# Kernel tuning notes

Measured on AMD Instinct MI355X. Metric: run time of the kernel, lower is better.

Reference implementation:

```python
import jax, jax.numpy as jnp
import numpy as np

B, S, H, E, K = 8, 4096, 1024, 256, 64
NEG = -1e30  # finite stand-in for -inf to keep grads NaN-free


def setup_inputs() -> dict:
    key = jax.random.key(0)
    ks = jax.random.split(key, 8)
    Hq = H // 4
    sc = 0.02
    return {
        "hidden_states": jax.random.normal(ks[0], (B, S, H), dtype=jnp.float32),
        "attention_mask": jnp.ones((B, S), dtype=jnp.int32),
        "block_boundaries": jnp.sort(jax.random.randint(ks[1], (B, K), 0, S), axis=-1),
        "tok_w1": jax.random.normal(ks[2], (H, Hq), dtype=jnp.float32) * sc,
        "tok_b1": jnp.zeros((Hq,), dtype=jnp.float32),
        "tok_w2": jax.random.normal(ks[3], (Hq, 1), dtype=jnp.float32) * sc,
        "tok_b2": jnp.zeros((1,), dtype=jnp.float32),
        "blk_w1": jax.random.normal(ks[4], (H, Hq), dtype=jnp.float32) * sc,
        "blk_b1": jnp.zeros((Hq,), dtype=jnp.float32),
        "blk_w2": jax.random.normal(ks[5], (Hq, 1), dtype=jnp.float32) * sc,
        "blk_b2": jnp.zeros((1,), dtype=jnp.float32),
        "out_w": jax.random.normal(ks[6], (H, E), dtype=jnp.float32) * sc,
        "out_b": jnp.zeros((E,), dtype=jnp.float32),
    }


def _attn_scores(x, w1, b1, w2, b2):
    # Linear -> Tanh -> Linear(.,1), squeeze last dim
    return (jnp.tanh(x @ w1 + b1) @ w2 + b2)[..., 0]


def reference(hidden_states, attention_mask, block_boundaries,
              tok_w1, tok_b1, tok_w2, tok_b2,
              blk_w1, blk_b1, blk_w2, blk_b2,
              out_w, out_b):
    Bz, Sz, Hz = hidden_states.shape
    Kz = block_boundaries.shape[1]
    pos = jnp.arange(Sz)
    # token -> block id: last boundary <= pos (tokens before first boundary get -1)
    block_id = jax.vmap(lambda bnd: jnp.searchsorted(bnd, pos, side='right') - 1)(block_boundaries)  # [B,S]
    member = block_id[:, :, None] == jnp.arange(Kz)[None, None, :]      # [B,S,K]
    valid = (attention_mask == 1) & (block_id >= 0)                     # [B,S]
    m_full = member & valid[:, :, None]                                 # [B,S,K]

    # stage 1: per-block masked softmax over tokens
    tok_scores = _attn_scores(hidden_states, tok_w1, tok_b1, tok_w2, tok_b2)  # [B,S]
    s = jnp.where(m_full, tok_scores[:, :, None], NEG)
    mx = jnp.max(s, axis=1, keepdims=True)                              # [B,1,K]
    e = jnp.where(m_full, jnp.exp(tok_scores[:, :, None] - mx), 0.0)
    denom = jnp.sum(e, axis=1, keepdims=True)                           # [B,1,K]
    w = jnp.where(denom > 0, e / jnp.maximum(denom, 1e-30), 0.0)
    block_embed = jnp.einsum('bsk,bsd->bkd', w, hidden_states)          # [B,K,H]
    block_valid = denom[:, 0, :] > 0                                    # [B,K] (empty blocks dropped)

    # stage 2: softmax over (non-empty) blocks
    blk_scores = _attn_scores(block_embed, blk_w1, blk_b1, blk_w2, blk_b2)    # [B,K]
    blk_scores = jnp.where(block_valid, blk_scores, NEG)
    bw = jax.nn.softmax(blk_scores, axis=-1)
    func = jnp.einsum('bk,bkd->bd', bw, block_embed)                    # [B,H]

    out = func @ out_w + out_b                                          # [B,E]
    return out / jnp.maximum(jnp.linalg.norm(out, axis=-1, keepdims=True), 1e-12)
```

## Files before the change

### kernel.cpp

```cpp
#include <hip/hip_runtime.h>
#include <math.h>
#include <limits.h>

#define BB 8
#define SS 4096
#define HH 1024
#define EE 256
#define KK 64
#define HQ 256
#define NEGF -1e30f

typedef short bf16x8 __attribute__((ext_vector_type(8)));
typedef float f32x4  __attribute__((ext_vector_type(4)));

__device__ inline short f2bf(float x) {
    unsigned u = __float_as_uint(x);
    unsigned r = (u + 0x7fffu + ((u >> 16) & 1u)) >> 16;
    return (short)r;
}

__device__ inline unsigned pk2bf(float lo, float hi) {
    unsigned a = __float_as_uint(lo) + 0x8000u;
    unsigned b = __float_as_uint(hi) + 0x8000u;
    return (a >> 16) | (b & 0xffff0000u);
}

__global__ __launch_bounds__(256) void convert_both_kernel(
    const float* __restrict__ tok_w1, const float* __restrict__ blk_w1,
    short* __restrict__ w1s_tok, short* __restrict__ w1s_blk)
{
    const int kb = blockIdx.x & 31, which = blockIdx.x >> 5;
    const float* src = which ? blk_w1 : tok_w1;
    short* dst = which ? w1s_blk : w1s_tok;
    const int n = threadIdx.x;
    for (int kk = 0; kk < 32; kk++)
        dst[kb * 8192 + n * 32 + kk] = f2bf(src[(kb * 32 + kk) * HQ + n]);
}

__global__ __launch_bounds__(256, 4) void mfma_score4_kernel(
    const float* __restrict__ X, const short* __restrict__ w1s,
    const float* __restrict__ b1, const float* __restrict__ w2,
    const float* __restrict__ b2, float* __restrict__ out)
{
    __shared__ __attribute__((aligned(16))) short As[2][1024];
    __shared__ float part[4][32];

    const int t = threadIdx.x;
    const int wv = t >> 6, lane = t & 63, lo = lane & 15, q = lane >> 4;
    const long row0 = (long)blockIdx.x * 32;

    f32x4 acc[2][4];
#pragma unroll
    for (int i = 0; i < 2; i++)
#pragma unroll
        for (int j = 0; j < 4; j++) acc[i][j] = (f32x4){0.f, 0.f, 0.f, 0.f};

    const int c = t >> 1, half = t & 1;
    const int srow = ((c >> 6) << 4) + (c & 15);
    const int skofs = ((c >> 4) & 3) * 8 + half * 4;
    const float* xs = X + (row0 + srow) * HH + skofs;
    short* const dst0 = &As[0][c * 8 + half * 4];
    short* const dst1 = &As[1][c * 8 + half * 4];
    const short* wp = w1s + (wv * 64 + lo) * 32 + q * 8;

    {
        float4 v = *(const float4*)xs;
        unsigned u0 = pk2bf(v.x, v.y), u1 = pk2bf(v.z, v.w);
        ((unsigned*)dst0)[0] = u0; ((unsigned*)dst0)[1] = u1;
    }
    bf16x8 bA[4], bB[4];
#pragma unroll
    for (int ct = 0; ct < 4; ct++)
        bA[ct] = *(const bf16x8*)(wp + ct * 512);
    __syncthreads();

    for (int kb = 0; kb < 32; kb += 2) {
        {
            float4 v = *(const float4*)(xs + (kb + 1) * 32);
#pragma unroll
            for (int ct = 0; ct < 4; ct++)
                bB[ct] = *(const bf16x8*)(wp + (kb + 1) * 8192 + ct * 512);
            bf16x8 af[2];
#pragma unroll
            for (int rt = 0; rt < 2; rt++)
                af[rt] = *(bf16x8*)(&As[0][(rt * 64 + q * 16 + lo) * 8]);
#pragma unroll
            for (int rt = 0; rt < 2; rt++)
#pragma unroll
                for (int ct = 0; ct < 4; ct++)
                    acc[rt][ct] = __builtin_amdgcn_mfma_f32_16x16x32_bf16(
                        af[rt], bA[ct], acc[rt][ct], 0, 0, 0);
            unsigned u0 = pk2bf(v.x, v.y), u1 = pk2bf(v.z, v.w);
            ((unsigned*)dst1)[0] = u0; ((unsigned*)dst1)[1] = u1;
        }
        __syncthreads();
        {
            const int k2 = (kb + 2 < 32) ? kb + 2 : 31;
            float4 v = *(const float4*)(xs + k2 * 32);
#pragma unroll
            for (int ct = 0; ct < 4; ct++)
                bA[ct] = *(const bf16x8*)(wp + k2 * 8192 + ct * 512);
            bf16x8 af[2];
#pragma unroll
            for (int rt = 0; rt < 2; rt++)
                af[rt] = *(bf16x8*)(&As[1][(rt * 64 + q * 16 + lo) * 8]);
#pragma unroll
            for (int rt = 0; rt < 2; rt++)
#pragma unroll
                for (int ct = 0; ct < 4; ct++)
                    acc[rt][ct] = __builtin_amdgcn_mfma_f32_16x16x32_bf16(
                        af[rt], bB[ct], acc[rt][ct], 0, 0, 0);
            unsigned u0 = pk2bf(v.x, v.y), u1 = pk2bf(v.z, v.w);
            ((unsigned*)dst0)[0] = u0; ((unsigned*)dst0)[1] = u1;
        }
        __syncthreads();
    }

    float rowpart[2][4];
#pragma unroll
    for (int rt = 0; rt < 2; rt++)
#pragma unroll
        for (int r = 0; r < 4; r++) rowpart[rt][r] = 0.f;
#pragma unroll
    for (int ct = 0; ct < 4; ct++) {
        const int cc = wv * 64 + ct * 16 + lo;
        const float b1c = b1[cc], w2c = w2[cc];
#pragma unroll
        for (int rt = 0; rt < 2; rt++)
#pragma unroll
            for (int r = 0; r < 4; r++)
                rowpart[rt][r] += tanhf(acc[rt][ct][r] + b1c) * w2c;
    }
#pragma unroll
    for (int rt = 0; rt < 2; rt++)
#pragma unroll
        for (int r = 0; r < 4; r++) {
            float v = rowpart[rt][r];
            v += __shfl_down(v, 8, 64);
            v += __shfl_down(v, 4, 64);
            v += __shfl_down(v, 2, 64);
            v += __shfl_down(v, 1, 64);
            rowpart[rt][r] = v;
        }
    if (lo == 0)
#pragma unroll
        for (int rt = 0; rt < 2; rt++)
#pragma unroll
            for (int r = 0; r < 4; r++)
                part[wv][rt * 16 + q * 4 + r] = rowpart[rt][r];
    __syncthreads();
    if (t < 32)
        out[row0 + t] = part[0][t] + part[1][t] + part[2][t] + part[3][t] + b2[0];
}

__global__ __launch_bounds__(256) void block_stats_kernel(
    const float* __restrict__ scores, const int* __restrict__ mask,
    const int* __restrict__ bnd, float* __restrict__ bden,
    float* __restrict__ wtok, float* __restrict__ embed)
{
    const int b = blockIdx.x >> 6, k = blockIdx.x & 63;
    const int start = bnd[b * KK + k];
    const int end = (k == KK - 1) ? SS : bnd[b * KK + k + 1];
    const int tid = threadIdx.x;
    __shared__ float r[4];
    __shared__ float mshared, dshared;

    *((float4*)(embed + (long)blockIdx.x * HH) + tid) = (float4){0.f, 0.f, 0.f, 0.f};
    if (k == 0)
        for (int s = tid; s < start; s += 256) wtok[b * SS + s] = 0.f;

    float m = NEGF;
    for (int s = start + tid; s < end; s += 256)
        if (mask[b * SS + s] == 1) m = fmaxf(m, scores[b * SS + s]);
    for (int off = 32; off > 0; off >>= 1) m = fmaxf(m, __shfl_down(m, off, 64));
    if ((tid & 63) == 0) r[tid >> 6] = m;
    __syncthreads();
    if (tid == 0) mshared = fmaxf(fmaxf(r[0], r[1]), fmaxf(r[2], r[3]));
    __syncthreads();
    m = mshared;

    float d = 0.f;
    for (int s = start + tid; s < end; s += 256)
        if (mask[b * SS + s] == 1) d += expf(scores[b * SS + s] - m);
    for (int off = 32; off > 0; off >>= 1) d += __shfl_down(d, off, 64);
    __syncthreads();
    if ((tid & 63) == 0) r[tid >> 6] = d;
    __syncthreads();
    if (tid == 0) {
        float den = r[0] + r[1] + r[2] + r[3];
        bden[blockIdx.x] = den;
        dshared = (den > 0.f) ? 1.f / fmaxf(den, 1e-30f) : 0.f;
    }
    __syncthreads();
    const float inv = dshared;
    for (int s = start + tid; s < end; s += 256)
        wtok[b * SS + s] = (mask[b * SS + s] == 1) ? expf(scores[b * SS + s] - m) * inv : 0.f;
}

#define TCH 16
__global__ __launch_bounds__(256) void block_embed4_kernel(
    const float* __restrict__ hidden, const float* __restrict__ wtok,
    const int* __restrict__ bnd, float* __restrict__ embed)
{
    const int b = blockIdx.x >> 8;
    const int ch = blockIdx.x & 255;
    const int t = threadIdx.x;
    __shared__ int bsh[KK];
    __shared__ float wsh[TCH];
    const int s0 = ch * TCH, s1 = s0 + TCH;
    if (t < KK) bsh[t] = bnd[b * KK + t];
    if (t >= 64 && t < 64 + TCH) wsh[t - 64] = wtok[b * SS + s0 + (t - 64)];
    __syncthreads();

    int cur = -1;
#pragma unroll
    for (int i = 0; i < KK; i++) cur = (bsh[i] <= s0) ? i : cur;
    const int nxt = (cur + 1 < KK) ? bsh[cur + 1] : INT_MAX;

    const float* hr0 = hidden + ((long)b * SS + s0) * HH + t;
    float a0 = 0.f, a1 = 0.f, a2 = 0.f, a3 = 0.f;

    if (nxt >= s1 && cur >= 0) {
#pragma unroll
        for (int i = 0; i < TCH; i++) {
            const float w = wsh[i];
            const float* hr = hr0 + (long)i * HH;
            a0 = fmaf(w, hr[0], a0);
            a1 = fmaf(w, hr[256], a1);
            a2 = fmaf(w, hr[512], a2);
            a3 = fmaf(w, hr[768], a3);
        }
        float* e = embed + ((long)b * KK + cur) * HH;
        atomicAdd(e + t, a0); atomicAdd(e + t + 256, a1);
        atomicAdd(e + t + 512, a2); atomicAdd(e + t + 768, a3);
        return;
    }

    bool any = false;
    for (int s = s0; s < s1; s++) {
        while (cur + 1 < KK && bsh[cur + 1] <= s) {
            if (any) {
                float* e = embed + ((long)b * KK + cur) * HH;
                atomicAdd(e + t, a0); atomicAdd(e + t + 256, a1);
                atomicAdd(e + t + 512, a2); atomicAdd(e + t + 768, a3);
                a0 = a1 = a2 = a3 = 0.f; any = false;
            }
            cur++;
        }
        if (cur < 0) continue;
        const float w = wsh[s - s0];
        const float* hr = hr0 + (long)(s - s0) * HH;
        a0 = fmaf(w, hr[0], a0);
        a1 = fmaf(w, hr[256], a1);
        a2 = fmaf(w, hr[512], a2);
        a3 = fmaf(w, hr[768], a3);
        any = true;
    }
    if (any) {
        float* e = embed + ((long)b * KK + cur) * HH;
        atomicAdd(e + t, a0); atomicAdd(e + t + 256, a1);
        atomicAdd(e + t + 512, a2); atomicAdd(e + t + 768, a3);
    }
}

__global__ __launch_bounds__(256) void finalize_ab_kernel(
    const float* __restrict__ embed, const float* __restrict__ bscores,
    const float* __restrict__ bden, const float* __restrict__ out_w,
    float* __restrict__ osum)
{
    const int b = blockIdx.x >> 3, hc = blockIdx.x & 7;
    const int t = threadIdx.x;
    __shared__ float bw[KK];
    __shared__ float fpart[2][128];
    __shared__ float fsh[128];

    if (t < KK) {
        float s = (bden[b * KK + t] > 0.f) ? bscores[b * KK + t] : NEGF;
        float m = s;
        for (int off = 32; off > 0; off >>= 1) m = fmaxf(m, __shfl_xor(m, off, 64));
        float e = expf(s - m);
        float d = e;
        for (int off = 32; off > 0; off >>= 1) d += __shfl_xor(d, off, 64);
        bw[t] = e / d;
    }
    __syncthreads();

    {
        const int hh = t & 127, kh = t >> 7;
        const float* ep = embed + ((long)b * KK + kh * 32) * HH + hc * 128 + hh;
        float f = 0.f;
#pragma unroll 8
        for (int k2 = 0; k2 < 32; k2++)
            f = fmaf(bw[kh * 32 + k2], ep[(long)k2 * HH], f);
        fpart[kh][hh] = f;
    }
    __syncthreads();
    if (t < 128) fsh[t] = fpart[0][t] + fpart[1][t];
    __syncthreads();

    float acc = 0.f;
    const float* wpp = out_w + (long)(hc * 128) * EE + t;
#pragma unroll 8
    for (int h = 0; h < 128; h++)
        acc = fmaf(fsh[h], wpp[(long)h * EE], acc);
    osum[(long)(b * 8 + hc) * EE + t] = acc;
}

__global__ __launch_bounds__(256) void finalize_c_kernel(
    const float* __restrict__ osum, const float* __restrict__ out_b,
    float* __restrict__ outp)
{
    const int b = blockIdx.x, t = threadIdx.x;
    __shared__ float r4[4];
    float o = out_b[t];
#pragma unroll
    for (int hc = 0; hc < 8; hc++)
        o += osum[(long)(b * 8 + hc) * EE + t];
    float sq = o * o;
    for (int off = 32; off > 0; off >>= 1) sq += __shfl_down(sq, off, 64);
    if ((t & 63) == 0) r4[t >> 6] = sq;
    __syncthreads();
    const float nrm = sqrtf(r4[0] + r4[1] + r4[2] + r4[3]);
    outp[b * EE + t] = o / fmaxf(nrm, 1e-12f);
}

extern "C" void kernel_launch(void* const* d_in, const int* in_sizes, int n_in,
                              void* d_out, int out_size, void* d_ws, size_t ws_size,
                              hipStream_t stream) {
    const float* hidden  = (const float*)d_in[0];
    const int*   mask    = (const int*)  d_in[1];
    const int*   bnd     = (const int*)  d_in[2];
    const float* tok_w1  = (const float*)d_in[3];
    const float* tok_b1  = (const float*)d_in[4];
    const float* tok_w2  = (const float*)d_in[5];
    const float* tok_b2  = (const float*)d_in[6];
    const float* blk_w1  = (const float*)d_in[7];
    const float* blk_b1  = (const float*)d_in[8];
    const float* blk_w2  = (const float*)d_in[9];
    const float* blk_b2  = (const float*)d_in[10];
    const float* out_w   = (const float*)d_in[11];
    const float* out_b   = (const float*)d_in[12];

    float* ws      = (float*)d_ws;
    float* wtok    = ws;
    float* embed   = ws + 32768;
    float* scores  = ws + 557056;
    float* bden    = ws + 589824;
    float* bscores = ws + 590336;
    float* osum    = ws + 590848;
    short* w1s_tok = (short*)(ws + 607232);
    short* w1s_blk = w1s_tok + 262144;

    convert_both_kernel<<<64, 256, 0, stream>>>(tok_w1, blk_w1, w1s_tok, w1s_blk);
    mfma_score4_kernel<<<BB * SS / 32, 256, 0, stream>>>(
        hidden, w1s_tok, tok_b1, tok_w2, tok_b2, scores);
    block_stats_kernel<<<BB * KK, 256, 0, stream>>>(
        scores, mask, bnd, bden, wtok, embed);
    block_embed4_kernel<<<BB * SS / TCH, 256, 0, stream>>>(hidden, wtok, bnd, embed);
    mfma_score4_kernel<<<BB * KK / 32, 256, 0, stream>>>(
        embed, w1s_blk, blk_b1, blk_w2, blk_b2, bscores);
    finalize_ab_kernel<<<BB * 8, 256, 0, stream>>>(
        embed, bscores, bden, out_w, osum);
    finalize_c_kernel<<<BB, 256, 0, stream>>>(osum, out_b, (float*)d_out);
}
```

Measured before the change: 302.5 us.

## Load X fragments directly into registers, dropping LDS staging and barriers

The score kernel no longer stages the bf16-converted X tile through shared memory with double buffering and __syncthreads. Each lane now loads its own MFMA A-fragment straight from global memory as fp32 float4 pairs and converts it to bf16 in registers, prefetching the next k-step. This removes LDS traffic and block-wide barriers. In exchange, all four waves redundantly load the same X rows (4x global/L2 reads of X), and register pressure rises.

```diff
diff --git a/kernel.cpp b/kernel.cpp
--- a/kernel.cpp
+++ b/kernel.cpp
@@ -42,7 +42,6 @@
     const float* __restrict__ b1, const float* __restrict__ w2,
     const float* __restrict__ b2, float* __restrict__ out)
 {
-    __shared__ __attribute__((aligned(16))) short As[2][1024];
     __shared__ float part[4][32];
 
     const int t = threadIdx.x;
@@ -55,65 +54,66 @@
 #pragma unroll
         for (int j = 0; j < 4; j++) acc[i][j] = (f32x4){0.f, 0.f, 0.f, 0.f};
 
-    const int c = t >> 1, half = t & 1;
-    const int srow = ((c >> 6) << 4) + (c & 15);
-    const int skofs = ((c >> 4) & 3) * 8 + half * 4;
-    const float* xs = X + (row0 + srow) * HH + skofs;
-    short* const dst0 = &As[0][c * 8 + half * 4];
-    short* const dst1 = &As[1][c * 8 + half * 4];
+    const float* xp0 = X + (row0 + lo) * HH + q * 8;
+    const float* xp1 = xp0 + 16 * HH;
     const short* wp = w1s + (wv * 64 + lo) * 32 + q * 8;
 
-    {
-        float4 v = *(const float4*)xs;
-        unsigned u0 = pk2bf(v.x, v.y), u1 = pk2bf(v.z, v.w);
-        ((unsigned*)dst0)[0] = u0; ((unsigned*)dst0)[1] = u1;
-    }
-    bf16x8 bA[4], bB[4];
+    float4 aC[2][2], aN[2][2];
+    bf16x8 bC[4], bN[4];
+
+    aC[0][0] = *(const float4*)(xp0);
+    aC[0][1] = *(const float4*)(xp0 + 4);
+    aC[1][0] = *(const float4*)(xp1);
+    aC[1][1] = *(const float4*)(xp1 + 4);
 #pragma unroll
     for (int ct = 0; ct < 4; ct++)
-        bA[ct] = *(const bf16x8*)(wp + ct * 512);
-    __syncthreads();
+        bC[ct] = *(const bf16x8*)(wp + ct * 512);
 
     for (int kb = 0; kb < 32; kb += 2) {
         {
-            float4 v = *(const float4*)(xs + (kb + 1) * 32);
+            const int kn = kb + 1;
+            aN[0][0] = *(const float4*)(xp0 + kn * 32);
+            aN[0][1] = *(const float4*)(xp0 + kn * 32 + 4);
+            aN[1][0] = *(const float4*)(xp1 + kn * 32);
+            aN[1][1] = *(const float4*)(xp1 + kn * 32 + 4);
 #pragma unroll
             for (int ct = 0; ct < 4; ct++)
-                bB[ct] = *(const bf16x8*)(wp + (kb + 1) * 8192 + ct * 512);
-            bf16x8 af[2];
-#pragma unroll
-            for (int rt = 0; rt < 2; rt++)
-                af[rt] = *(bf16x8*)(&As[0][(rt * 64 + q * 16 + lo) * 8]);
-#pragma unroll
-            for (int rt = 0; rt < 2; rt++)
+                bN[ct] = *(const bf16x8*)(wp + kn * 8192 + ct * 512);
+#pragma unroll
+            for (int rt = 0; rt < 2; rt++) {
+                union { unsigned u[4]; bf16x8 v; } af;
+                af.u[0] = pk2bf(aC[rt][0].x, aC[rt][0].y);
+                af.u[1] = pk2bf(aC[rt][0].z, aC[rt][0].w);
+                af.u[2] = pk2bf(aC[rt][1].x, aC[rt][1].y);
+                af.u[3] = pk2bf(aC[rt][1].z, aC[rt][1].w);
 #pragma unroll
                 for (int ct = 0; ct < 4; ct++)
                     acc[rt][ct] = __builtin_amdgcn_mfma_f32_16x16x32_bf16(
-                        af[rt], bA[ct], acc[rt][ct], 0, 0, 0);
-            unsigned u0 = pk2bf(v.x, v.y), u1 = pk2bf(v.z, v.w);
-            ((unsigned*)dst1)[0] = u0; ((unsigned*)dst1)[1] = u1;
-        }
-        __syncthreads();
+                        af.v, bC[ct], acc[rt][ct], 0, 0, 0);
+            }
+        }
         {
-            const int k2 = (kb + 2 < 32) ? kb + 2 : 31;
-            float4 v = *(const float4*)(xs + k2 * 32);
+            const int kn = (kb + 2 < 32) ? kb + 2 : 31;
+            aC[0][0] = *(const float4*)(xp0 + kn * 32);
+            aC[0][1] = *(const float4*)(xp0 + kn * 32 + 4);
+            aC[1][0] = *(const float4*)(xp1 + kn * 32);
+            aC[1][1] = *(const float4*)(xp1 + kn * 32 + 4);
 #pragma unroll
             for (int ct = 0; ct < 4; ct++)
-                bA[ct] = *(const bf16x8*)(wp + k2 * 8192 + ct * 512);
-            bf16x8 af[2];
-#pragma unroll
-            for (int rt = 0; rt < 2; rt++)
-                af[rt] = *(bf16x8*)(&As[1][(rt * 64 + q * 16 + lo) * 8]);
-#pragma unroll
-            for (int rt = 0; rt < 2; rt++)
+                bC[ct] = *(const bf16x8*)(wp + kn * 8192 + ct * 512);
+#pragma unroll
+            for (int rt = 0; rt < 2; rt++) {
+                union { unsigned u[4]; bf16x8 v; } af;
+                af.u[0] = pk2bf(aN[rt][0].x, aN[rt][0].y);
+                af.u[1] = pk2bf(aN[rt][0].z, aN[rt][0].w);
+                af.u[2] = pk2bf(aN[rt][1].x, aN[rt][1].y);
+                af.u[3] = pk2bf(aN[rt][1].z, aN[rt][1].w);
 #pragma unroll
                 for (int ct = 0; ct < 4; ct++)
                     acc[rt][ct] = __builtin_amdgcn_mfma_f32_16x16x32_bf16(
-                        af[rt], bB[ct], acc[rt][ct], 0, 0, 0);
-            unsigned u0 = pk2bf(v.x, v.y), u1 = pk2bf(v.z, v.w);
-            ((unsigned*)dst0)[0] = u0; ((unsigned*)dst0)[1] = u1;
-        }
-        __syncthreads();
+                        af.v, bN[ct], acc[rt][ct], 0, 0, 0);
+            }
+        }
     }
 
     float rowpart[2][4];
```

Measured after the change: 389.4 us. +28.7%, slower.

## Stage four k-slices per barrier in the MFMA score kernel with deeper prefetch

Applied to the files above, without the earlier changes.

Restructures the token-score GEMM main loop so each shared-memory stage holds four 32-wide k-slices instead of one. Barriers drop from one per slice to one per four slices, and X prefetch runs two stages ahead using four float4 registers. Manual lgkmcnt waits and sched_barriers replace __syncthreads. The cost is four times the LDS, which may reduce occupancy at 4 blocks/CU, plus extra registers for the prefetched values.

```diff
diff --git a/kernel.cpp b/kernel.cpp
--- a/kernel.cpp
+++ b/kernel.cpp
@@ -42,7 +42,7 @@
     const float* __restrict__ b1, const float* __restrict__ w2,
     const float* __restrict__ b2, float* __restrict__ out)
 {
-    __shared__ __attribute__((aligned(16))) short As[2][1024];
+    __shared__ __attribute__((aligned(16))) short As[2][4][1024];
     __shared__ float part[4][32];
 
     const int t = threadIdx.x;
@@ -59,62 +59,71 @@
     const int srow = ((c >> 6) << 4) + (c & 15);
     const int skofs = ((c >> 4) & 3) * 8 + half * 4;
     const float* xs = X + (row0 + srow) * HH + skofs;
-    short* const dst0 = &As[0][c * 8 + half * 4];
-    short* const dst1 = &As[1][c * 8 + half * 4];
+    const int dofs = c * 8 + half * 4;
     const short* wp = w1s + (wv * 64 + lo) * 32 + q * 8;
 
-    {
-        float4 v = *(const float4*)xs;
-        unsigned u0 = pk2bf(v.x, v.y), u1 = pk2bf(v.z, v.w);
-        ((unsigned*)dst0)[0] = u0; ((unsigned*)dst0)[1] = u1;
-    }
-    bf16x8 bA[4], bB[4];
-#pragma unroll
-    for (int ct = 0; ct < 4; ct++)
-        bA[ct] = *(const bf16x8*)(wp + ct * 512);
-    __syncthreads();
-
-    for (int kb = 0; kb < 32; kb += 2) {
-        {
-            float4 v = *(const float4*)(xs + (kb + 1) * 32);
-#pragma unroll
-            for (int ct = 0; ct < 4; ct++)
-                bB[ct] = *(const bf16x8*)(wp + (kb + 1) * 8192 + ct * 512);
-            bf16x8 af[2];
-#pragma unroll
-            for (int rt = 0; rt < 2; rt++)
-                af[rt] = *(bf16x8*)(&As[0][(rt * 64 + q * 16 + lo) * 8]);
-#pragma unroll
-            for (int rt = 0; rt < 2; rt++)
-#pragma unroll
-                for (int ct = 0; ct < 4; ct++)
-                    acc[rt][ct] = __builtin_amdgcn_mfma_f32_16x16x32_bf16(
-                        af[rt], bA[ct], acc[rt][ct], 0, 0, 0);
-            unsigned u0 = pk2bf(v.x, v.y), u1 = pk2bf(v.z, v.w);
-            ((unsigned*)dst1)[0] = u0; ((unsigned*)dst1)[1] = u1;
+    float4 sv[4];
+    bf16x8 bC[4], bN[4];
+
+#pragma unroll
+    for (int j = 0; j < 4; j++) sv[j] = *(const float4*)(xs + j * 32);
+#pragma unroll
+    for (int j = 0; j < 4; j++) {
+        unsigned u0 = pk2bf(sv[j].x, sv[j].y), u1 = pk2bf(sv[j].z, sv[j].w);
+        unsigned* d = (unsigned*)&As[0][j][dofs];
+        d[0] = u0; d[1] = u1;
+    }
+#pragma unroll
+    for (int j = 0; j < 4; j++) sv[j] = *(const float4*)(xs + (4 + j) * 32);
+#pragma unroll
+    for (int ct = 0; ct < 4; ct++) bC[ct] = *(const bf16x8*)(wp + ct * 512);
+    asm volatile("s_waitcnt lgkmcnt(0)" ::: "memory");
+    __builtin_amdgcn_sched_barrier(0);
+    __builtin_amdgcn_s_barrier();
+    __builtin_amdgcn_sched_barrier(0);
+
+#define KSTEP(J, BUSE, BPRE, KBN)                                              \
+    {                                                                          \
+        _Pragma("unroll")                                                      \
+        for (int ct = 0; ct < 4; ct++)                                         \
+            BPRE[ct] = *(const bf16x8*)(wp + (KBN) * 8192 + ct * 512);         \
+        bf16x8 af0 = *(const bf16x8*)&As[cur][J][(q * 16 + lo) * 8];           \
+        bf16x8 af1 = *(const bf16x8*)&As[cur][J][(64 + q * 16 + lo) * 8];      \
+        _Pragma("unroll")                                                      \
+        for (int ct = 0; ct < 4; ct++) {                                       \
+            acc[0][ct] = __builtin_amdgcn_mfma_f32_16x16x32_bf16(              \
+                af0, BUSE[ct], acc[0][ct], 0, 0, 0);                           \
+            acc[1][ct] = __builtin_amdgcn_mfma_f32_16x16x32_bf16(              \
+                af1, BUSE[ct], acc[1][ct], 0, 0, 0);                           \
+        }                                                                      \
+    }
+
+    for (int ci = 0; ci < 8; ci++) {
+        const int cur = ci & 1;
+        const int kb0 = ci * 4;
+        KSTEP(0, bC, bN, kb0 + 1)
+        KSTEP(1, bN, bC, kb0 + 2)
+        KSTEP(2, bC, bN, kb0 + 3)
+        const int kbn3 = (kb0 + 4 < 32) ? kb0 + 4 : 31;
+        KSTEP(3, bN, bC, kbn3)
+        if (ci < 7) {
+#pragma unroll
+            for (int j = 0; j < 4; j++) {
+                unsigned u0 = pk2bf(sv[j].x, sv[j].y), u1 = pk2bf(sv[j].z, sv[j].w);
+                unsigned* d = (unsigned*)&As[cur ^ 1][j][dofs];
+                d[0] = u0; d[1] = u1;
+            }
+            const int cn = (ci + 2 < 8) ? ci + 2 : 7;
+#pragma unroll
+            for (int j = 0; j < 4; j++)
+                sv[j] = *(const float4*)(xs + (cn * 4 + j) * 32);
         }
-        __syncthreads();
-        {
-            const int k2 = (kb + 2 < 32) ? kb + 2 : 31;
-            float4 v = *(const float4*)(xs + k2 * 32);
-#pragma unroll
-            for (int ct = 0; ct < 4; ct++)
-                bA[ct] = *(const bf16x8*)(wp + k2 * 8192 + ct * 512);
-            bf16x8 af[2];
-#pragma unroll
-            for (int rt = 0; rt < 2; rt++)
-                af[rt] = *(bf16x8*)(&As[1][(rt * 64 + q * 16 + lo) * 8]);
-#pragma unroll
-            for (int rt = 0; rt < 2; rt++)
-#pragma unroll
-                for (int ct = 0; ct < 4; ct++)
-                    acc[rt][ct] = __builtin_amdgcn_mfma_f32_16x16x32_bf16(
-                        af[rt], bB[ct], acc[rt][ct], 0, 0, 0);
-            unsigned u0 = pk2bf(v.x, v.y), u1 = pk2bf(v.z, v.w);
-            ((unsigned*)dst0)[0] = u0; ((unsigned*)dst0)[1] = u1;
-        }
-        __syncthreads();
-    }
+        asm volatile("s_waitcnt lgkmcnt(0)" ::: "memory");
+        __builtin_amdgcn_sched_barrier(0);
+        __builtin_amdgcn_s_barrier();
+        __builtin_amdgcn_sched_barrier(0);
+    }
+#undef KSTEP
 
     float rowpart[2][4];
 #pragma unroll
```

Result: no change. 297.1 us (-1.8%).

## Stage whole 32-row activation tile in LDS up front, drop per-step barriers

Applied to the files above, without the earlier changes.

The score kernel no longer double-buffers 32-column slices of X with a barrier every step. Each block now loads its full 32x1024 tile with wide, coalesced nontemporal loads, converts it to bf16 into 64KB of LDS, and syncs once. It then runs all MFMAs from LDS while prefetching the weight fragments four k-steps ahead in registers. The aim is better streaming of the large hidden_states read and fewer syncs. In exchange it uses more LDS and registers (occupancy hint cut to 2 blocks) and loses overlap between loading and compute within a block.

```diff
diff --git a/kernel.cpp b/kernel.cpp
--- a/kernel.cpp
+++ b/kernel.cpp
@@ -37,13 +37,14 @@
         dst[kb * 8192 + n * 32 + kk] = f2bf(src[(kb * 32 + kk) * HQ + n]);
 }
 
-__global__ __launch_bounds__(256, 4) void mfma_score4_kernel(
+__global__ __launch_bounds__(256, 2) void mfma_score32L_kernel(
     const float* __restrict__ X, const short* __restrict__ w1s,
     const float* __restrict__ b1, const float* __restrict__ w2,
     const float* __restrict__ b2, float* __restrict__ out)
 {
-    __shared__ __attribute__((aligned(16))) short As[2][1024];
+    __shared__ __attribute__((aligned(16))) short As[32][1024];
     __shared__ float part[4][32];
+    short* const AsF = &As[0][0];
 
     const int t = threadIdx.x;
     const int wv = t >> 6, lane = t & 63, lo = lane & 15, q = lane >> 4;
@@ -55,65 +56,67 @@
 #pragma unroll
         for (int j = 0; j < 4; j++) acc[i][j] = (f32x4){0.f, 0.f, 0.f, 0.f};
 
-    const int c = t >> 1, half = t & 1;
-    const int srow = ((c >> 6) << 4) + (c & 15);
-    const int skofs = ((c >> 4) & 3) * 8 + half * 4;
-    const float* xs = X + (row0 + srow) * HH + skofs;
-    short* const dst0 = &As[0][c * 8 + half * 4];
-    short* const dst1 = &As[1][c * 8 + half * 4];
     const short* wp = w1s + (wv * 64 + lo) * 32 + q * 8;
-
-    {
-        float4 v = *(const float4*)xs;
-        unsigned u0 = pk2bf(v.x, v.y), u1 = pk2bf(v.z, v.w);
-        ((unsigned*)dst0)[0] = u0; ((unsigned*)dst0)[1] = u1;
-    }
-    bf16x8 bA[4], bB[4];
-#pragma unroll
-    for (int ct = 0; ct < 4; ct++)
-        bA[ct] = *(const bf16x8*)(wp + ct * 512);
-    __syncthreads();
-
-    for (int kb = 0; kb < 32; kb += 2) {
-        {
-            float4 v = *(const float4*)(xs + (kb + 1) * 32);
+    bf16x8 bR[4][4];
+#pragma unroll
+    for (int kk = 0; kk < 4; kk++)
+#pragma unroll
+        for (int ct = 0; ct < 4; ct++)
+            bR[kk][ct] = *(const bf16x8*)(wp + kk * 8192 + ct * 512);
+
+    const int tconst = ((t >> 3) << 10) + (((t >> 1) & 3) << 7) + ((t & 1) << 2);
+    const float* xt = X + row0 * HH + 4 * t;
+
+    f32x4 va[8], vb[8];
+#pragma unroll
+    for (int j = 0; j < 8; j++)
+        va[j] = __builtin_nontemporal_load((const f32x4*)(xt + j * HH));
+#pragma unroll
+    for (int j = 0; j < 8; j++)
+        vb[j] = __builtin_nontemporal_load((const f32x4*)(xt + (8 + j) * HH));
+
+#define STASH(ROW, V)                                                          \
+    {                                                                          \
+        const int idx_ = tconst + (((ROW) >> 4) << 9) + (((ROW) & 15) << 3);   \
+        uint2 u_; u_.x = pk2bf((V).x, (V).y); u_.y = pk2bf((V).z, (V).w);      \
+        *(uint2*)&AsF[idx_] = u_;                                              \
+    }
+
+#pragma unroll
+    for (int j = 0; j < 8; j++) STASH(j, va[j])
+#pragma unroll
+    for (int j = 0; j < 8; j++)
+        va[j] = __builtin_nontemporal_load((const f32x4*)(xt + (16 + j) * HH));
+#pragma unroll
+    for (int j = 0; j < 8; j++) STASH(8 + j, vb[j])
+#pragma unroll
+    for (int j = 0; j < 8; j++)
+        vb[j] = __builtin_nontemporal_load((const f32x4*)(xt + (24 + j) * HH));
+#pragma unroll
+    for (int j = 0; j < 8; j++) STASH(16 + j, va[j])
+#pragma unroll
+    for (int j = 0; j < 8; j++) STASH(24 + j, vb[j])
+#undef STASH
+    __syncthreads();
+
+    for (int cb = 0; cb < 8; cb++) {
+#pragma unroll
+        for (int jj = 0; jj < 4; jj++) {
+            const int kb = cb * 4 + jj;
+            const bf16x8 af0 = *(const bf16x8*)&AsF[(kb << 10) + ((q * 16 + lo) << 3)];
+            const bf16x8 af1 = *(const bf16x8*)&AsF[(kb << 10) + ((64 + q * 16 + lo) << 3)];
+#pragma unroll
+            for (int ct = 0; ct < 4; ct++) {
+                acc[0][ct] = __builtin_amdgcn_mfma_f32_16x16x32_bf16(
+                    af0, bR[jj][ct], acc[0][ct], 0, 0, 0);
+                acc[1][ct] = __builtin_amdgcn_mfma_f32_16x16x32_bf16(
+                    af1, bR[jj][ct], acc[1][ct], 0, 0, 0);
+            }
+            const int kn = (kb + 4 < 32) ? kb + 4 : 31;
 #pragma unroll
             for (int ct = 0; ct < 4; ct++)
-                bB[ct] = *(const bf16x8*)(wp + (kb + 1) * 8192 + ct * 512);
-            bf16x8 af[2];
-#pragma unroll
-            for (int rt = 0; rt < 2; rt++)
-                af[rt] = *(bf16x8*)(&As[0][(rt * 64 + q * 16 + lo) * 8]);
-#pragma unroll
-            for (int rt = 0; rt < 2; rt++)
-#pragma unroll
-                for (int ct = 0; ct < 4; ct++)
-                    acc[rt][ct] = __builtin_amdgcn_mfma_f32_16x16x32_bf16(
-                        af[rt], bA[ct], acc[rt][ct], 0, 0, 0);
-            unsigned u0 = pk2bf(v.x, v.y), u1 = pk2bf(v.z, v.w);
-            ((unsigned*)dst1)[0] = u0; ((unsigned*)dst1)[1] = u1;
+                bR[jj][ct] = *(const bf16x8*)(wp + kn * 8192 + ct * 512);
         }
-        __syncthreads();
-        {
-            const int k2 = (kb + 2 < 32) ? kb + 2 : 31;
-            float4 v = *(const float4*)(xs + k2 * 32);
-#pragma unroll
-            for (int ct = 0; ct < 4; ct++)
-                bA[ct] = *(const bf16x8*)(wp + k2 * 8192 + ct * 512);
-            bf16x8 af[2];
-#pragma unroll
-            for (int rt = 0; rt < 2; rt++)
-                af[rt] = *(bf16x8*)(&As[1][(rt * 64 + q * 16 + lo) * 8]);
-#pragma unroll
-            for (int rt = 0; rt < 2; rt++)
-#pragma unroll
-                for (int ct = 0; ct < 4; ct++)
-                    acc[rt][ct] = __builtin_amdgcn_mfma_f32_16x16x32_bf16(
-                        af[rt], bB[ct], acc[rt][ct], 0, 0, 0);
-            unsigned u0 = pk2bf(v.x, v.y), u1 = pk2bf(v.z, v.w);
-            ((unsigned*)dst0)[0] = u0; ((unsigned*)dst0)[1] = u1;
-        }
-        __syncthreads();
     }
 
     float rowpart[2][4];
@@ -352,12 +355,12 @@
     short* w1s_blk = w1s_tok + 262144;
 
     convert_both_kernel<<<64, 256, 0, stream>>>(tok_w1, blk_w1, w1s_tok, w1s_blk);
-    mfma_score4_kernel<<<BB * SS / 32, 256, 0, stream>>>(
+    mfma_score32L_kernel<<<BB * SS / 32, 256, 0, stream>>>(
         hidden, w1s_tok, tok_b1, tok_w2, tok_b2, scores);
     block_stats_kernel<<<BB * KK, 256, 0, stream>>>(
         scores, mask, bnd, bden, wtok, embed);
     block_embed4_kernel<<<BB * SS / TCH, 256, 0, stream>>>(hidden, wtok, bnd, embed);
-    mfma_score4_kernel<<<BB * KK / 32, 256, 0, stream>>>(
+    mfma_score32L_kernel<<<BB * KK / 32, 256, 0, stream>>>(
         embed, w1s_blk, blk_b1, blk_w2, blk_b2, bscores);
     finalize_ab_kernel<<<BB * 8, 256, 0, stream>>>(
         embed, bscores, bden, out_w, osum);
```

New measurement: 318.0 us. 1.05x slower.
